# Performance work log

Measured on AMD Instinct MI355X. Metric: run time of the kernel, lower is better.

## Reference

```python
import jax, jax.numpy as jnp
import numpy as np

B, N, F_IN, F_OUT = 16, 2048, 512, 512


def setup_inputs() -> dict:
    key = jax.random.key(0)
    k1, k2, k3 = jax.random.split(key, 3)
    x = jax.random.normal(k1, (B, N, F_IN), dtype=jnp.float32)
    adj = jax.random.uniform(k2, (N, N), dtype=jnp.float32)
    # Kaiming uniform fan_out: bound = sqrt(6 / fan_out)
    bound = np.sqrt(6.0 / F_OUT)
    weight = jax.random.uniform(k3, (F_IN, F_OUT), dtype=jnp.float32,
                                minval=-bound, maxval=bound)
    bias = jnp.zeros((F_OUT,), dtype=jnp.float32)
    return {"x": x, "adj": adj, "weight": weight, "bias": bias}


def reference(x, adj, weight, bias):
    # Symmetric degree normalization: D^{-1/2} A D^{-1/2}
    deg = adj.sum(axis=1)                                   # [N]
    deg_inv_sqrt = jnp.where(deg > 0, jax.lax.rsqrt(deg), 0.0)
    # row/column rescale instead of diag matmuls (same math, O(N^2))
    norm_adj = adj * deg_inv_sqrt[:, None] * deg_inv_sqrt[None, :]
    support = jnp.einsum('bni,io->bno', x, weight)          # [B,N,F_OUT]
    output = jnp.einsum('nm,bmo->bno', norm_adj, support)   # [B,N,F_OUT]
    return output + bias
```

## Files before the change

### kernel.cpp

```cpp
#include <hip/hip_runtime.h>
#include <stdint.h>

typedef __attribute__((ext_vector_type(8))) __bf16 bf16x8;
typedef __attribute__((ext_vector_type(4))) float f32x4;
typedef unsigned short u16;

__device__ __forceinline__ u16 f2bf(float f) {
  unsigned u = __builtin_bit_cast(unsigned, f);
  unsigned r = 0x7FFFu + ((u >> 16) & 1u);
  return (u16)((u + r) >> 16);
}

__device__ __forceinline__ void gload16(const void* g, void* l) {
  __builtin_amdgcn_global_load_lds(
      (__attribute__((address_space(1))) void*)(g),
      (__attribute__((address_space(3))) void*)(l),
      16, 0, 0);
}

__global__ void row_deg_k(const float* __restrict__ adj, float* __restrict__ dis, int N) {
  int row = blockIdx.x;
  const float4* a = (const float4*)(adj + (size_t)row * N);
  float s = 0.f;
  for (int j = threadIdx.x; j < N / 4; j += 256) {
    float4 v = a[j];
    s += v.x + v.y + v.z + v.w;
  }
#pragma unroll
  for (int off = 32; off > 0; off >>= 1) s += __shfl_down(s, off, 64);
  __shared__ float wsum[4];
  if ((threadIdx.x & 63) == 0) wsum[threadIdx.x >> 6] = s;
  __syncthreads();
  if (threadIdx.x == 0) {
    float t = wsum[0] + wsum[1] + wsum[2] + wsum[3];
    dis[row] = (t > 0.f) ? (1.0f / sqrtf(t)) : 0.f;
  }
}

__global__ void conv_bf16_k(const float* __restrict__ in, u16* __restrict__ o, int n4) {
  int i = blockIdx.x * 256 + threadIdx.x;
  if (i >= n4) return;
  float4 v = ((const float4*)in)[i];
  ushort4 u;
  u.x = f2bf(v.x); u.y = f2bf(v.y); u.z = f2bf(v.z); u.w = f2bf(v.w);
  ((ushort4*)o)[i] = u;
}

__global__ void conv_wt_k(const float* __restrict__ w, u16* __restrict__ wt) {
  int idx = blockIdx.x * 256 + threadIdx.x;
  int i = idx >> 9, o = idx & 511;
  wt[o * 512 + i] = f2bf(w[idx]);
}

__global__ void make_nadj_k(const float* __restrict__ adj, const float* __restrict__ dis,
                            u16* __restrict__ o, int N) {
  int idx = blockIdx.x * 256 + threadIdx.x;
  int i = idx >> 9;
  int j4 = (idx & 511) * 4;
  float di = dis[i];
  float4 a = ((const float4*)adj)[idx];
  ushort4 u;
  u.x = f2bf(a.x * di * dis[j4 + 0]);
  u.y = f2bf(a.y * di * dis[j4 + 1]);
  u.z = f2bf(a.z * di * dis[j4 + 2]);
  u.w = f2bf(a.w * di * dis[j4 + 3]);
  ((ushort4*)o)[idx] = u;
}

template <int EPI>
__launch_bounds__(512, 2)
__global__ void gemm256_k(const u16* __restrict__ A, int lda,
                          const u16* __restrict__ Bt, int ldb,
                          void* __restrict__ Cv, int ldc,
                          const float* __restrict__ bias, int K,
                          int nMT, int nNT, size_t zBt, size_t zC) {
  __shared__ __align__(16) u16 lds[65536];

  const int tid = threadIdx.x;
  const int lane = tid & 63;
  const int wid = tid >> 6;
  const int wr = wid >> 2;
  const int wc = wid & 3;

  const int flat = blockIdx.x;
  const int wg = (flat & 7) * ((int)gridDim.x >> 3) + (flat >> 3);
  const int m_t = wg % nMT;
  const int rest = wg / nMT;
  const int n_t = rest % nNT;
  const int b = rest / nNT;
  const int rowBase = m_t * 256;
  const int colBase = n_t * 256;
  const u16* Bb = Bt + (size_t)b * zBt;

  const int lr = tid >> 3;
  const int kkl = (tid & 7) * 8;
  const int kswz = kkl ^ ((lr & 7) << 3);
  const u16* gA = A + (size_t)(rowBase + lr) * lda + kswz;
  const u16* gB = Bb + (size_t)(colBase + lr) * ldb + kswz;
  u16* lA = lds + lr * 64 + kkl;
  u16* lB = lds + 32768 + lr * 64 + kkl;

  const int fr = lane & 15;
  const int rswz = (lane & 7) << 3;
  const int kp0 = ((lane >> 4) * 8) ^ rswz;
  const int kp1 = (32 | ((lane >> 4) * 8)) ^ rswz;
  const u16* fA = lds + (wr * 128 + fr) * 64;
  const u16* fB = lds + 32768 + (wc * 64 + fr) * 64;

  f32x4 acc[8][4] = {};
  bf16x8 a0[4], a1[4], b0[4], b1[4];

  const int NT = K >> 6;

#define STAGE_A(d, h, t)                                                             \
  do {                                                                               \
    gload16(gA + (size_t)((h) * 64) * lda + (size_t)(t) * 64,                        \
            lA + (d) * 16384 + ((h) * 64) * 64);                                     \
    gload16(gA + (size_t)((h) * 64 + 128) * lda + (size_t)(t) * 64,                  \
            lA + (d) * 16384 + ((h) * 64 + 128) * 64);                               \
  } while (0)

#define STAGE_B(d, h, t)                                                             \
  do {                                                                               \
    gload16(gB + (size_t)((h) * 128) * ldb + (size_t)(t) * 64,                       \
            lB + (d) * 16384 + ((h) * 128) * 64);                                    \
    gload16(gB + (size_t)((h) * 128 + 64) * ldb + (size_t)(t) * 64,                  \
            lB + (d) * 16384 + ((h) * 128 + 64) * 64);                               \
  } while (0)

#define RD_A8(mh, c)                                                                 \
  _Pragma("unroll") for (int m = 0; m < 4; ++m) {                                    \
    a0[m] = *(const bf16x8*)(fA + (c) * 16384 + (mh) * 4096 + m * 1024 + kp0);       \
    a1[m] = *(const bf16x8*)(fA + (c) * 16384 + (mh) * 4096 + m * 1024 + kp1);       \
  }

#define RD_B4(nlo, c)                                                                \
  _Pragma("unroll") for (int n = 0; n < 2; ++n) {                                    \
    b0[(nlo) + n] = *(const bf16x8*)(fB + (c) * 16384 + ((nlo) + n) * 1024 + kp0);   \
    b1[(nlo) + n] = *(const bf16x8*)(fB + (c) * 16384 + ((nlo) + n) * 1024 + kp1);   \
  }

#define PRE()                                                                        \
  __builtin_amdgcn_sched_barrier(0);                                                 \
  __builtin_amdgcn_s_barrier();                                                      \
  asm volatile("s_waitcnt lgkmcnt(0)" ::: "memory");                                 \
  __builtin_amdgcn_sched_barrier(0);                                                 \
  __builtin_amdgcn_s_setprio(1)

#define POST()                                                                       \
  __builtin_amdgcn_s_setprio(0);                                                     \
  __builtin_amdgcn_sched_barrier(0)

#define MFMA_Q(mh, nlo)                                                              \
  _Pragma("unroll") for (int m = 0; m < 4; ++m) {                                    \
    _Pragma("unroll") for (int n = 0; n < 2; ++n) {                                  \
      acc[(mh) * 4 + m][(nlo) + n] = __builtin_amdgcn_mfma_f32_16x16x32_bf16(        \
          a0[m], b0[(nlo) + n], acc[(mh) * 4 + m][(nlo) + n], 0, 0, 0);              \
      acc[(mh) * 4 + m][(nlo) + n] = __builtin_amdgcn_mfma_f32_16x16x32_bf16(        \
          a1[m], b1[(nlo) + n], acc[(mh) * 4 + m][(nlo) + n], 0, 0, 0);              \
    }                                                                                \
  }

  {
    const int t1 = (NT > 1) ? 1 : 0;
    STAGE_A(0, 0, 0);
    STAGE_B(0, 0, 0);
    STAGE_B(0, 1, 0);
    STAGE_A(0, 1, 0);
    STAGE_A(1, 0, t1);
    STAGE_B(1, 0, t1);
    STAGE_A(1, 1, t1);
    asm volatile("s_waitcnt vmcnt(6)" ::: "memory");
    __builtin_amdgcn_s_barrier();
  }

  for (int t = 0; t < NT; ++t) {
    const int c = t & 1;
    const int cn = c ^ 1;
    const int tB1 = (t + 1 < NT) ? t + 1 : NT - 1;
    const int t2 = (t + 2 < NT) ? t + 2 : NT - 1;

    RD_A8(0, c);
    RD_B4(0, c);
    STAGE_B(cn, 1, tB1);
    asm volatile("s_waitcnt lgkmcnt(8)" ::: "memory");
    PRE();
    MFMA_Q(0, 0);
    POST();
    __builtin_amdgcn_s_barrier();

    RD_B4(2, c);
    STAGE_A(c, 0, t2);
    PRE();
    MFMA_Q(0, 2);
    POST();
    asm volatile("s_waitcnt vmcnt(12)" ::: "memory");
    __builtin_amdgcn_s_barrier();

    RD_A8(1, c);
    STAGE_B(c, 0, t2);
    PRE();
    MFMA_Q(1, 2);
    POST();
    __builtin_amdgcn_s_barrier();

    STAGE_A(c, 1, t2);
    PRE();
    MFMA_Q(1, 0);
    POST();
    asm volatile("s_waitcnt vmcnt(6)" ::: "memory");
    __builtin_amdgcn_s_barrier();
  }
  asm volatile("s_waitcnt vmcnt(0)" ::: "memory");

  if (EPI == 0) {
    u16* C = (u16*)Cv;
#pragma unroll
    for (int am = 0; am < 8; ++am) {
      const int r = rowBase + wr * 128 + (am >> 2) * 64 + (am & 3) * 16 + (lane >> 4) * 4;
#pragma unroll
      for (int n = 0; n < 4; ++n) {
        const int cc = colBase + wc * 64 + n * 16 + (lane & 15);
        ushort4 v;
        v.x = f2bf(acc[am][n][0]);
        v.y = f2bf(acc[am][n][1]);
        v.z = f2bf(acc[am][n][2]);
        v.w = f2bf(acc[am][n][3]);
        *reinterpret_cast<ushort4*>(&C[(size_t)cc * ldc + r]) = v;
      }
    }
  } else {
    float* C = (float*)Cv + (size_t)b * zC;
#pragma unroll
    for (int n = 0; n < 4; ++n) {
      const int cc = colBase + wc * 64 + n * 16 + (lane & 15);
      const float bv = bias[cc];
#pragma unroll
      for (int am = 0; am < 8; ++am) {
        const int r = rowBase + wr * 128 + (am >> 2) * 64 + (am & 3) * 16 + (lane >> 4) * 4;
#pragma unroll
        for (int j = 0; j < 4; ++j)
          C[(size_t)(r + j) * ldc + cc] = acc[am][n][j] + bv;
      }
    }
  }
#undef STAGE_A
#undef STAGE_B
#undef RD_A8
#undef RD_B4
#undef PRE
#undef POST
#undef MFMA_Q
}

extern "C" void kernel_launch(void* const* d_in, const int* in_sizes, int n_in,
                              void* d_out, int out_size, void* d_ws, size_t ws_size,
                              hipStream_t stream) {
  const int B = 16, N = 2048, FIN = 512, FOUT = 512;
  const float* x    = (const float*)d_in[0];
  const float* adj  = (const float*)d_in[1];
  const float* w    = (const float*)d_in[2];
  const float* bias = (const float*)d_in[3];
  float* out = (float*)d_out;
  char* ws = (char*)d_ws;

  float* dis = (float*)ws;
  u16* wt    = (u16*)(ws + 8192);
  u16* nadj  = (u16*)(ws + 532480);
  u16* xb    = (u16*)(ws + 8921088);
  u16* st    = (u16*)(ws + 42475520);

  row_deg_k<<<N, 256, 0, stream>>>(adj, dis, N);
  conv_bf16_k<<<(B * N * FIN / 4 + 255) / 256, 256, 0, stream>>>(x, xb, B * N * FIN / 4);
  conv_wt_k<<<(FIN * FOUT) / 256, 256, 0, stream>>>(w, wt);
  make_nadj_k<<<(N * N / 4) / 256, 256, 0, stream>>>(adj, dis, nadj, N);

  gemm256_k<0><<<dim3(256), 512, 0, stream>>>(
      xb, FIN, wt, FIN, st, B * N, nullptr, FIN, 128, 2, 0, 0);

  gemm256_k<1><<<dim3(256), 512, 0, stream>>>(
      nadj, N, st, B * N, out, FOUT, bias, N, 8, 2,
      (size_t)N, (size_t)N * FOUT);
}
```

Before: 127.3 us.

## Unroll GEMM main loop by two with static buffer indices and reordered staging

The main K loop of the bf16 GEMM is unrolled by two so the LDS double-buffer indices become compile-time constants, and the order of global-to-LDS staging loads across the four MFMA quarters is reshuffled. The sched_barrier fences around each MFMA block are removed, which lets the compiler interleave instructions more freely. The vmcnt wait thresholds change to match the new issue order. The aim is less address arithmetic and better overlap of loads with MFMA, at the cost of more code size. It also assumes NT is even, and the changed wait counts risk ordering hazards.

```diff
diff --git a/kernel.cpp b/kernel.cpp
--- a/kernel.cpp
+++ b/kernel.cpp
@@ -111,6 +111,7 @@
   bf16x8 a0[4], a1[4], b0[4], b1[4];
 
   const int NT = K >> 6;
+  const int NI = NT >> 1;
 
 #define STAGE_A(d, h, t)                                                             \
   do {                                                                               \
@@ -140,18 +141,8 @@
     b1[(nlo) + n] = *(const bf16x8*)(fB + (c) * 16384 + ((nlo) + n) * 1024 + kp1);   \
   }
 
-#define PRE()                                                                        \
-  __builtin_amdgcn_sched_barrier(0);                                                 \
-  __builtin_amdgcn_s_barrier();                                                      \
-  asm volatile("s_waitcnt lgkmcnt(0)" ::: "memory");                                 \
-  __builtin_amdgcn_sched_barrier(0);                                                 \
-  __builtin_amdgcn_s_setprio(1)
-
-#define POST()                                                                       \
-  __builtin_amdgcn_s_setprio(0);                                                     \
-  __builtin_amdgcn_sched_barrier(0)
-
-#define MFMA_Q(mh, nlo)                                                              \
+#define MFMA16(mh, nlo)                                                              \
+  __builtin_amdgcn_s_setprio(1);                                                     \
   _Pragma("unroll") for (int m = 0; m < 4; ++m) {                                    \
     _Pragma("unroll") for (int n = 0; n < 2; ++n) {                                  \
       acc[(mh) * 4 + m][(nlo) + n] = __builtin_amdgcn_mfma_f32_16x16x32_bf16(        \
@@ -159,7 +150,13 @@
       acc[(mh) * 4 + m][(nlo) + n] = __builtin_amdgcn_mfma_f32_16x16x32_bf16(        \
           a1[m], b1[(nlo) + n], acc[(mh) * 4 + m][(nlo) + n], 0, 0, 0);              \
     }                                                                                \
-  }
+  }                                                                                  \
+  __builtin_amdgcn_s_setprio(0)
+
+#define LGKM0() asm volatile("s_waitcnt lgkmcnt(0)" ::: "memory")
+#define LGKM8() asm volatile("s_waitcnt lgkmcnt(8)" ::: "memory")
+#define VM6()   asm volatile("s_waitcnt vmcnt(6)" ::: "memory")
+#define BAR()   __builtin_amdgcn_s_barrier()
 
   {
     const int t1 = (NT > 1) ? 1 : 0;
@@ -169,47 +166,67 @@
     STAGE_A(0, 1, 0);
     STAGE_A(1, 0, t1);
     STAGE_B(1, 0, t1);
+    STAGE_B(1, 1, t1);
+    VM6();
+    BAR();
+  }
+
+  for (int i = 0; i < NI; ++i) {
+    const int t1 = 2 * i + 1;
+    const int s2 = (2 * i + 2 < NT) ? 2 * i + 2 : NT - 1;
+    const int s3 = (2 * i + 3 < NT) ? 2 * i + 3 : NT - 1;
+
+    RD_A8(0, 0);
+    RD_B4(0, 0);
     STAGE_A(1, 1, t1);
-    asm volatile("s_waitcnt vmcnt(6)" ::: "memory");
-    __builtin_amdgcn_s_barrier();
-  }
-
-  for (int t = 0; t < NT; ++t) {
-    const int c = t & 1;
-    const int cn = c ^ 1;
-    const int tB1 = (t + 1 < NT) ? t + 1 : NT - 1;
-    const int t2 = (t + 2 < NT) ? t + 2 : NT - 1;
-
-    RD_A8(0, c);
-    RD_B4(0, c);
-    STAGE_B(cn, 1, tB1);
-    asm volatile("s_waitcnt lgkmcnt(8)" ::: "memory");
-    PRE();
-    MFMA_Q(0, 0);
-    POST();
-    __builtin_amdgcn_s_barrier();
-
-    RD_B4(2, c);
-    STAGE_A(c, 0, t2);
-    PRE();
-    MFMA_Q(0, 2);
-    POST();
-    asm volatile("s_waitcnt vmcnt(12)" ::: "memory");
-    __builtin_amdgcn_s_barrier();
-
-    RD_A8(1, c);
-    STAGE_B(c, 0, t2);
-    PRE();
-    MFMA_Q(1, 2);
-    POST();
-    __builtin_amdgcn_s_barrier();
-
-    STAGE_A(c, 1, t2);
-    PRE();
-    MFMA_Q(1, 0);
-    POST();
-    asm volatile("s_waitcnt vmcnt(6)" ::: "memory");
-    __builtin_amdgcn_s_barrier();
+    LGKM8();
+    BAR(); LGKM0();
+    MFMA16(0, 0);
+    BAR();
+
+    RD_B4(2, 0);
+    STAGE_A(0, 0, s2);
+    BAR(); LGKM0();
+    MFMA16(0, 2);
+    BAR();
+
+    RD_A8(1, 0);
+    STAGE_B(0, 0, s2);
+    BAR(); LGKM0();
+    MFMA16(1, 2);
+    BAR();
+
+    STAGE_B(0, 1, s2);
+    BAR(); LGKM0();
+    MFMA16(1, 0);
+    VM6();
+    BAR();
+
+    RD_A8(0, 1);
+    RD_B4(0, 1);
+    STAGE_A(0, 1, s2);
+    LGKM8();
+    BAR(); LGKM0();
+    MFMA16(0, 0);
+    BAR();
+
+    RD_B4(2, 1);
+    STAGE_A(1, 0, s3);
+    BAR(); LGKM0();
+    MFMA16(0, 2);
+    BAR();
+
+    RD_A8(1, 1);
+    STAGE_B(1, 0, s3);
+    BAR(); LGKM0();
+    MFMA16(1, 2);
+    BAR();
+
+    STAGE_B(1, 1, s3);
+    BAR(); LGKM0();
+    MFMA16(1, 0);
+    VM6();
+    BAR();
   }
   asm volatile("s_waitcnt vmcnt(0)" ::: "memory");
 
@@ -248,9 +265,11 @@
 #undef STAGE_B
 #undef RD_A8
 #undef RD_B4
-#undef PRE
-#undef POST
-#undef MFMA_Q
+#undef MFMA16
+#undef LGKM0
+#undef LGKM8
+#undef VM6
+#undef BAR
 }
 
 extern "C" void kernel_launch(void* const* d_in, const int* in_sizes, int n_in,
```

After: 124.5 us. 1.02x faster.
